# Performance work log

Measured on AMD Instinct MI355X. Metric: run time of the kernel, lower is better.

Reference implementation:

```python
import jax, jax.numpy as jnp
import numpy as np

N, D, K = 262144, 64, 512


def setup_inputs() -> dict:
    key = jax.random.key(0)
    k1, k2 = jax.random.split(key)
    x = jax.random.normal(k1, (N, D), dtype=jnp.float32)
    # embedding initialized uniform(-1/K, 1/K) as in the torch module
    codebook = jax.random.uniform(k2, (K, D), dtype=jnp.float32, minval=-1.0 / K, maxval=1.0 / K)
    return {"x": x, "codebook": codebook}


def reference(x, codebook):
    # distances[n,k] = ||x_n||^2 + ||w_k||^2 - 2 x_n . w_k  (cdist^2 via matmul)
    d = (jnp.sum(x * x, axis=1, keepdims=True)
         + jnp.sum(codebook * codebook, axis=1)
         - 2.0 * jnp.matmul(x, codebook.T))  # [N, K]
    indices = jnp.argmin(d, axis=1)          # [N]
    x_q = codebook[indices]                  # [N, D] gather
    commitment_loss = jnp.mean((jax.lax.stop_gradient(x_q) - x) ** 2)
    embedding_loss = jnp.mean((x_q - jax.lax.stop_gradient(x)) ** 2)
    vq_loss = commitment_loss * 0.25 + embedding_loss
    # straight-through estimator
    x_out = x + jax.lax.stop_gradient(x_q - x)
    return (x_out, vq_loss)
```

## Files before the change

### kernel.cpp

```cpp
#include <hip/hip_runtime.h>

#define N_ROWS 262144
#define DIM    64
#define KCB    512

#define MBLOCKS  512
#define MTHREADS 512

typedef float f32x4 __attribute__((ext_vector_type(4)));

__device__ inline float dot4(float4 a) {
    return a.x * a.x + a.y * a.y + a.z * a.z + a.w * a.w;
}

__device__ inline long pk8(float4 f0, float4 f1, float s) {
    int lo = 0, hi = 0;
    lo = __builtin_amdgcn_cvt_pk_fp8_f32(f0.x * s, f0.y * s, lo, false);
    lo = __builtin_amdgcn_cvt_pk_fp8_f32(f0.z * s, f0.w * s, lo, true);
    hi = __builtin_amdgcn_cvt_pk_fp8_f32(f1.x * s, f1.y * s, hi, false);
    hi = __builtin_amdgcn_cvt_pk_fp8_f32(f1.z * s, f1.w * s, hi, true);
    return (long)(((unsigned long)(unsigned)hi << 32) | (unsigned)lo);
}

__device__ inline float packmin(f32x4 acc, unsigned kb, float run) {
    const unsigned mask = 0xFFFFFE00u;
    float p0 = __uint_as_float((__float_as_uint(acc[0]) & mask) | kb);
    float p1 = __uint_as_float((__float_as_uint(acc[1]) & mask) | (kb | 1u));
    float p2 = __uint_as_float((__float_as_uint(acc[2]) & mask) | (kb | 2u));
    float p3 = __uint_as_float((__float_as_uint(acc[3]) & mask) | (kb | 3u));
    return fminf(fminf(fminf(p0, p1), p2), fminf(run, p3));
}

__global__ void vq_prep(const float* __restrict__ cb, long* __restrict__ cb8,
                        float* __restrict__ wn) {
    const int fg  = blockIdx.x * 512 + threadIdx.x;
    const int row = fg >> 3, g = fg & 7;
    const float* src = cb + row * DIM + g * 8;
    float4 f0 = *(const float4*)src;
    float4 f1 = *(const float4*)(src + 4);
    float sq = dot4(f0) + dot4(f1);
    sq += __shfl_xor(sq, 1);
    sq += __shfl_xor(sq, 2);
    sq += __shfl_xor(sq, 4);
    const int slot = ((row >> 1) << 4) + ((row & 1) << 3)
                   + (g ^ ((row >> 1) & 7));
    cb8[slot] = pk8(f0, f1, -256.0f);
    if (g == 0) wn[row] = 256.0f + 128.0f * sq;
}

__global__ __launch_bounds__(MTHREADS, 2) void vq_main(
    const float* __restrict__ x, const float* __restrict__ cb,
    const f32x4* __restrict__ img_g, float* __restrict__ out,
    float* __restrict__ partials)
{
    __shared__ f32x4 img[2176];
    __shared__ float red_sh[8];

    const int tid    = threadIdx.x;
    const int lane   = tid & 63;
    const int wave   = tid >> 6;
    const int lane15 = lane & 15;
    const int half   = lane >> 4;

    const int wrow = blockIdx.x * 512 + wave * 64;
    const float* xc = x + (size_t)(wrow + lane15) * DIM + half * 8;

    float4 a[4][4];
    #pragma unroll
    for (int c = 0; c < 4; ++c) {
        const float* xp = xc + c * 1024;
        a[c][0] = *(const float4*)xp;        a[c][1] = *(const float4*)(xp + 4);
        a[c][2] = *(const float4*)(xp + 32); a[c][3] = *(const float4*)(xp + 36);
    }

    #pragma unroll
    for (int it = 0; it < 4; ++it)
        img[tid + it * 512] = img_g[tid + it * 512];
    if (tid < 128) img[2048 + tid] = img_g[2048 + tid];

    float xn[4];
    long  blo[4], bhi[4];
    #pragma unroll
    for (int c = 0; c < 4; ++c) {
        xn[c]  = dot4(a[c][0]) + dot4(a[c][1]) + dot4(a[c][2]) + dot4(a[c][3]);
        blo[c] = pk8(a[c][0], a[c][1], 1.0f);
        bhi[c] = pk8(a[c][2], a[c][3], 1.0f);
    }
    __syncthreads();

    const long*  cb8 = (const long*)img;
    const f32x4* wn4 = img + 2048;

    const int key  = (lane15 >> 1) & 7;
    const int base = (lane15 >> 1) * 16 + (lane15 & 1) * 8;
    const int slo  = base + (half ^ key);
    const int shi  = slo ^ 4;
    const unsigned hb   = (unsigned)(half * 4);
    const unsigned mask = 0xFFFFFE00u;

    float run0 = __uint_as_float(0x7F7FFFFFu);
    float run1 = run0, run2 = run0, run3 = run0;

    #pragma unroll 4
    for (int t = 0; t < 32; ++t) {
        long  alo = cb8[t * 128 + slo];
        long  ahi = cb8[t * 128 + shi];
        f32x4 wnv = wn4[t * 4 + half];
        const unsigned kb = (unsigned)(t * 16) | hb;

        f32x4 c0 = wnv;
        c0 = __builtin_amdgcn_mfma_f32_16x16x32_fp8_fp8(alo, blo[0], c0, 0, 0, 0);
        c0 = __builtin_amdgcn_mfma_f32_16x16x32_fp8_fp8(ahi, bhi[0], c0, 0, 0, 0);
        run0 = packmin(c0, kb, run0);

        f32x4 c1 = wnv;
        c1 = __builtin_amdgcn_mfma_f32_16x16x32_fp8_fp8(alo, blo[1], c1, 0, 0, 0);
        c1 = __builtin_amdgcn_mfma_f32_16x16x32_fp8_fp8(ahi, bhi[1], c1, 0, 0, 0);
        run1 = packmin(c1, kb, run1);

        f32x4 c2 = wnv;
        c2 = __builtin_amdgcn_mfma_f32_16x16x32_fp8_fp8(alo, blo[2], c2, 0, 0, 0);
        c2 = __builtin_amdgcn_mfma_f32_16x16x32_fp8_fp8(ahi, bhi[2], c2, 0, 0, 0);
        run2 = packmin(c2, kb, run2);

        f32x4 c3 = wnv;
        c3 = __builtin_amdgcn_mfma_f32_16x16x32_fp8_fp8(alo, blo[3], c3, 0, 0, 0);
        c3 = __builtin_amdgcn_mfma_f32_16x16x32_fp8_fp8(ahi, bhi[3], c3, 0, 0, 0);
        run3 = packmin(c3, kb, run3);
    }

    float runs[4] = {run0, run1, run2, run3};
    float lossAcc = 0.f;
    #pragma unroll
    for (int c = 0; c < 4; ++c) {
        float r = runs[c];
        r = fminf(r, __shfl_xor(r, 16));
        r = fminf(r, __shfl_xor(r, 32));
        float xs = xn[c];
        xs += __shfl_xor(xs, 16); xs += __shfl_xor(xs, 32);

        const unsigned f0 = __float_as_uint(r);
        float pf = __uint_as_float(f0 & mask);
        lossAcc += 0.25f * (xs + pf * (1.0f / 128.0f) - 2.0f);
        const int bk0 = (int)(f0 & 511u);

        float* outw = out + (size_t)(wrow + c * 16) * DIM;
        #pragma unroll
        for (int j = 0; j < 4; ++j) {
            const int srcl = (j * 4 + half) & 15;
            int bk = __shfl(bk0, srcl);
            f32x4 qv = *(const f32x4*)(cb + (size_t)bk * DIM + lane15 * 4);
            *(f32x4*)(outw + j * 256 + lane * 4) = qv;
        }
    }

    #pragma unroll
    for (int off = 1; off < 64; off <<= 1) lossAcc += __shfl_xor(lossAcc, off);
    if (lane == 0) red_sh[wave] = lossAcc;
    __syncthreads();
    if (tid == 0) {
        float s = 0.f;
        #pragma unroll
        for (int w = 0; w < 8; ++w) s += red_sh[w];
        partials[blockIdx.x] = s;
    }
}

__global__ void vq_finalize(const float* __restrict__ partials,
                            float* __restrict__ out_loss) {
    __shared__ float sh[256];
    int t = threadIdx.x;
    sh[t] = partials[t] + partials[t + 256];
    __syncthreads();
    #pragma unroll
    for (int s = 128; s > 0; s >>= 1) {
        if (t < s) sh[t] += sh[t + s];
        __syncthreads();
    }
    if (t == 0) out_loss[0] = sh[0] * (1.25f / (float)(N_ROWS * DIM));
}

extern "C" void kernel_launch(void* const* d_in, const int* in_sizes, int n_in,
                              void* d_out, int out_size, void* d_ws, size_t ws_size,
                              hipStream_t stream) {
    const float* x  = (const float*)d_in[0];
    const float* cb = (const float*)d_in[1];
    float* out      = (float*)d_out;
    long*  ws_cb8   = (long*)d_ws;
    float* ws_wn    = (float*)((char*)d_ws + 32768);
    float* partials = (float*)((char*)d_ws + 36864);

    hipLaunchKernelGGL(vq_prep, dim3(8), dim3(512), 0, stream, cb, ws_cb8, ws_wn);
    hipLaunchKernelGGL(vq_main, dim3(MBLOCKS), dim3(MTHREADS), 0, stream,
                       x, cb, (const f32x4*)d_ws, out, partials);
    hipLaunchKernelGGL(vq_finalize, dim3(1), dim3(256), 0, stream,
                       partials, out + (size_t)N_ROWS * DIM);
}
```

Before: 39.27 us.

## Split scoring and codebook gather into separate kernels via index buffer

Moves the output gather out of the scoring kernel: the scoring kernel now writes a 16-bit argmin index per row to workspace, and a new lightweight gather kernel reads those indices and writes the quantized rows with fully coalesced float4 stores. The aim is to keep the MFMA scoring kernel free of the long tail of gather loads and stores, and to let the gather run at high occupancy. In exchange it adds an extra kernel launch and an index round-trip through global memory. It also adds a compiler memory barrier after the x loads.

```diff
diff --git a/kernel.cpp b/kernel.cpp
--- a/kernel.cpp
+++ b/kernel.cpp
@@ -4,8 +4,10 @@
 #define DIM    64
 #define KCB    512
 
-#define MBLOCKS  512
-#define MTHREADS 512
+#define ABLOCKS  512
+#define ATHREADS 512
+#define BTHREADS 256
+#define BBLOCKS  ((N_ROWS * 16) / BTHREADS)
 
 typedef float f32x4 __attribute__((ext_vector_type(4)));
 
@@ -48,10 +50,9 @@
     if (g == 0) wn[row] = 256.0f + 128.0f * sq;
 }
 
-__global__ __launch_bounds__(MTHREADS, 2) void vq_main(
-    const float* __restrict__ x, const float* __restrict__ cb,
-    const f32x4* __restrict__ img_g, float* __restrict__ out,
-    float* __restrict__ partials)
+__global__ __launch_bounds__(ATHREADS, 2) void vq_score(
+    const float* __restrict__ x, const f32x4* __restrict__ img_g,
+    unsigned short* __restrict__ idx, float* __restrict__ partials)
 {
     __shared__ f32x4 img[2176];
     __shared__ float red_sh[8];
@@ -72,6 +73,7 @@
         a[c][0] = *(const float4*)xp;        a[c][1] = *(const float4*)(xp + 4);
         a[c][2] = *(const float4*)(xp + 32); a[c][3] = *(const float4*)(xp + 36);
     }
+    asm volatile("" ::: "memory");
 
     #pragma unroll
     for (int it = 0; it < 4; ++it)
@@ -142,16 +144,9 @@
         const unsigned f0 = __float_as_uint(r);
         float pf = __uint_as_float(f0 & mask);
         lossAcc += 0.25f * (xs + pf * (1.0f / 128.0f) - 2.0f);
-        const int bk0 = (int)(f0 & 511u);
-
-        float* outw = out + (size_t)(wrow + c * 16) * DIM;
-        #pragma unroll
-        for (int j = 0; j < 4; ++j) {
-            const int srcl = (j * 4 + half) & 15;
-            int bk = __shfl(bk0, srcl);
-            f32x4 qv = *(const f32x4*)(cb + (size_t)bk * DIM + lane15 * 4);
-            *(f32x4*)(outw + j * 256 + lane * 4) = qv;
-        }
+
+        if (lane < 16)
+            idx[wrow + c * 16 + lane] = (unsigned short)(f0 & 511u);
     }
 
     #pragma unroll
@@ -164,6 +159,18 @@
         for (int w = 0; w < 8; ++w) s += red_sh[w];
         partials[blockIdx.x] = s;
     }
+}
+
+__global__ __launch_bounds__(BTHREADS, 8) void vq_gather(
+    const unsigned short* __restrict__ idx, const float* __restrict__ cb,
+    float* __restrict__ out)
+{
+    const int g   = blockIdx.x * BTHREADS + threadIdx.x;
+    const int row = g >> 4;
+    const int dq  = g & 15;
+    const int k   = (int)idx[row];
+    const f32x4* cb4 = (const f32x4*)cb;
+    ((f32x4*)out)[g] = cb4[k * 16 + dq];
 }
 
 __global__ void vq_finalize(const float* __restrict__ partials,
@@ -189,10 +196,13 @@
     long*  ws_cb8   = (long*)d_ws;
     float* ws_wn    = (float*)((char*)d_ws + 32768);
     float* partials = (float*)((char*)d_ws + 36864);
+    unsigned short* idx = (unsigned short*)((char*)d_ws + 40960);
 
     hipLaunchKernelGGL(vq_prep, dim3(8), dim3(512), 0, stream, cb, ws_cb8, ws_wn);
-    hipLaunchKernelGGL(vq_main, dim3(MBLOCKS), dim3(MTHREADS), 0, stream,
-                       x, cb, (const f32x4*)d_ws, out, partials);
+    hipLaunchKernelGGL(vq_score, dim3(ABLOCKS), dim3(ATHREADS), 0, stream,
+                       x, (const f32x4*)d_ws, idx, partials);
+    hipLaunchKernelGGL(vq_gather, dim3(BBLOCKS), dim3(BTHREADS), 0, stream,
+                       idx, cb, out);
     hipLaunchKernelGGL(vq_finalize, dim3(1), dim3(256), 0, stream,
                        partials, out + (size_t)N_ROWS * DIM);
 }
```

After: 48.64 us. 23.9% more time.
